# Kernel tuning notes

Hardware: AMD Instinct MI355X
Metric: run time of the kernel (lower is better)

## Reference

```python
import jax, jax.numpy as jnp
import numpy as np

B, C, F = 16384, 1000, 256
ALPHA = 10


def setup_inputs() -> dict:
    key = jax.random.key(0)
    k1, k2, k3, k4, k5 = jax.random.split(key, 5)
    logits = jax.random.normal(k1, (B, C), dtype=jnp.float32)
    features = jax.random.normal(k2, (B, F), dtype=jnp.float32)
    mean_vecs = jax.random.normal(k3, (C, F), dtype=jnp.float32)
    # Per-class Weibull (shape, loc, scale) as fit by scipy.weibull_min.fit.
    wb_shape = jax.random.uniform(k4, (C,), dtype=jnp.float32, minval=1.0, maxval=4.0)
    wb_loc = jnp.zeros((C,), dtype=jnp.float32)
    # typical tail distance for randn features/means is ~sqrt(2F) ~ 22.6
    wb_scale = jax.random.uniform(k5, (C,), dtype=jnp.float32, minval=10.0, maxval=25.0)
    return {"logits": logits, "features": features, "mean_vecs": mean_vecs,
            "wb_shape": wb_shape, "wb_loc": wb_loc, "wb_scale": wb_scale}


def reference(logits, features, mean_vecs, wb_shape, wb_loc, wb_scale):
    # Batched per-class Euclidean distances via the GEMM identity
    # ||f - m||^2 = ||f||^2 + ||m||^2 - 2 f.m  (avoids [B,C,F] intermediate).
    f2 = jnp.sum(features * features, axis=1, keepdims=True)        # [B,1]
    m2 = jnp.sum(mean_vecs * mean_vecs, axis=1)                     # [C]
    d2 = f2 + m2[None, :] - 2.0 * (features @ mean_vecs.T)          # [B,C]
    dist = jnp.sqrt(jnp.maximum(d2, 1e-12))                         # [B,C]
    # Analytic weibull_min CDF: 1 - exp(-((x - loc)/scale)^c), 0 for x <= loc.
    xp = (dist - wb_loc[None, :]) / wb_scale[None, :]
    pos = xp > 0
    xp_safe = jnp.where(pos, xp, 1.0)
    w = jnp.where(pos, 1.0 - jnp.exp(-(xp_safe ** wb_shape[None, :])), 0.0)
    # OpenMax reweighting + softmax (exp/sum-normalize as in the original).
    scores = logits * (1.0 - w ** ALPHA)                            # [B,C]
    return jax.nn.softmax(scores, axis=-1)
```

## Files before the change

### kernel.cpp

```cpp
#include <hip/hip_runtime.h>

#define NB 16384
#define NC 1000
#define NF 256
#define SE_STRIDE 1004

typedef _Float16 half8 __attribute__((ext_vector_type(8)));
typedef float f32x4 __attribute__((ext_vector_type(4)));

__global__ __launch_bounds__(256) void prep_kernel(
    const float* __restrict__ mean_vecs,
    const float* __restrict__ wb_shape,
    const float* __restrict__ wb_loc,
    const float* __restrict__ wb_scale,
    _Float16* __restrict__ m16f,
    float* __restrict__ pm2,
    float* __restrict__ psh,
    float* __restrict__ pli,
    float* __restrict__ pis)
{
    const int lane = threadIdx.x & 63;
    const int W = blockIdx.x * 4 + (threadIdx.x >> 6);

    if (W < 512) {
        const int gt = W >> 3, kk = W & 7;
        int cls = gt * 16 + (lane & 15);
        if (cls > NC - 1) cls = NC - 1;
        const float* src = mean_vecs + (size_t)cls * NF + kk * 32 + (lane >> 4) * 8;
        const float4 lo = *(const float4*)src;
        const float4 hi = *(const float4*)(src + 4);
        half8 h;
        h[0]=(_Float16)lo.x; h[1]=(_Float16)lo.y; h[2]=(_Float16)lo.z; h[3]=(_Float16)lo.w;
        h[4]=(_Float16)hi.x; h[5]=(_Float16)hi.y; h[6]=(_Float16)hi.z; h[7]=(_Float16)hi.w;
        *((half8*)m16f + (size_t)W * 64 + lane) = h;
    }
    if (W < NC) {
        const float4 v = *((const float4*)(mean_vecs + (size_t)W * NF) + lane);
        float s = v.x*v.x + v.y*v.y + v.z*v.z + v.w*v.w;
        #pragma unroll
        for (int off = 1; off < 64; off <<= 1) s += __shfl_xor(s, off, 64);
        if (lane == 0) {
            const float isc = 1.0f / wb_scale[W];
            pm2[W] = s;
            psh[W] = wb_shape[W];
            pli[W] = wb_loc[W] * isc;
            pis[W] = isc;
        }
    }
}

__global__ __launch_bounds__(512, 4) void score_kernel(
    const float* __restrict__ logits,
    const float* __restrict__ features,
    const _Float16* __restrict__ m16f,
    const float* __restrict__ pm2,
    const float* __restrict__ psh,
    const float* __restrict__ pli,
    const float* __restrict__ pis,
    float* __restrict__ out)
{
    __shared__ float se[16][SE_STRIDE];

    const int lane = threadIdx.x & 63;
    const int wave = threadIdx.x >> 6;
    const int q    = lane >> 4;
    const int mr   = lane & 15;
    const int row  = blockIdx.x * 16 + mr;

    const half8* mbase = (const half8*)m16f + (size_t)(wave * 8) * 8 * 64 + lane;

    half8 a[8];
    #pragma unroll
    for (int kk = 0; kk < 8; ++kk)
        a[kk] = mbase[kk * 64];

    half8 bfrag[8];
    float f2 = 0.f;
    const float* fb = features + (size_t)row * NF;
    #pragma unroll
    for (int kk = 0; kk < 8; ++kk) {
        const float4* p = (const float4*)(fb + kk * 32 + q * 8);
        const float4 lo = p[0], hi = p[1];
        f2 += lo.x*lo.x + lo.y*lo.y + lo.z*lo.z + lo.w*lo.w
            + hi.x*hi.x + hi.y*hi.y + hi.z*hi.z + hi.w*hi.w;
        half8 b;
        b[0]=(_Float16)lo.x; b[1]=(_Float16)lo.y; b[2]=(_Float16)lo.z; b[3]=(_Float16)lo.w;
        b[4]=(_Float16)hi.x; b[5]=(_Float16)hi.y; b[6]=(_Float16)hi.z; b[7]=(_Float16)hi.w;
        bfrag[kk] = b;
    }
    f2 += __shfl_xor(f2, 16, 64);
    f2 += __shfl_xor(f2, 32, 64);

    const float LOG2E = 1.44269504088896340736f;

    #pragma unroll
    for (int t = 0; t < 8; ++t) {
        const int gt   = wave * 8 + t;
        const int cb   = gt * 16 + q * 4;
        const bool cvg = (cb <= NC - 4);
        const int cbc  = cvg ? cb : (NC - 4);

        f32x4 acc = {0.f, 0.f, 0.f, 0.f};
        #pragma unroll
        for (int kk = 0; kk < 8; ++kk)
            acc = __builtin_amdgcn_mfma_f32_16x16x32_f16(a[kk], bfrag[kk], acc, 0, 0, 0);

        if (t < 7) {
            #pragma unroll
            for (int kk = 0; kk < 8; ++kk)
                a[kk] = mbase[(size_t)((t + 1) * 8 + kk) * 64];
        }

        const float4 m2v = *(const float4*)(pm2 + cbc);
        const float4 shv = *(const float4*)(psh + cbc);
        const float4 liv = *(const float4*)(pli + cbc);
        const float4 iv  = *(const float4*)(pis + cbc);

        const float* m2a = (const float*)&m2v;
        const float* sha = (const float*)&shv;
        const float* lia = (const float*)&liv;
        const float* iva = (const float*)&iv;

        f32x4 o;
        #pragma unroll
        for (int j = 0; j < 4; ++j) {
            float d2   = fmaxf(f2 + m2a[j] - 2.0f * acc[j], 1e-12f);
            float dist = sqrtf(d2);
            float xp   = dist * iva[j] - lia[j];
            float xs   = fmaxf(xp, 1e-30f);
            float tt   = exp2f(sha[j] * log2f(xs));
            float w    = 1.0f - exp2f(-LOG2E * tt);
            w = (xp > 0.f) ? w : 0.f;
            float w2 = w * w, w4 = w2 * w2, w8 = w4 * w4;
            o[j] = 1.0f - w8 * w2;
        }

        if (cvg)
            *(f32x4*)&se[mr][cb] = o;
    }

    __syncthreads();

    #pragma unroll
    for (int rr = 0; rr < 2; ++rr) {
        const int r = wave * 2 + rr;
        const size_t grow = (size_t)(blockIdx.x * 16 + r);
        const float* lrow = logits + grow * NC;

        float4 ev[4];
        float psum = 0.f;
        #pragma unroll
        for (int i = 0; i < 4; ++i) {
            const int idx = i * 64 + lane;
            if (idx < 250) {
                const float4 g4 = *(const float4*)&se[r][idx * 4];
                const float4 l4 = *(const float4*)(lrow + idx * 4);
                float4 e4;
                e4.x = exp2f(LOG2E * (l4.x * g4.x));
                e4.y = exp2f(LOG2E * (l4.y * g4.y));
                e4.z = exp2f(LOG2E * (l4.z * g4.z));
                e4.w = exp2f(LOG2E * (l4.w * g4.w));
                ev[i] = e4;
                psum += (e4.x + e4.y) + (e4.z + e4.w);
            }
        }
        #pragma unroll
        for (int off = 1; off < 64; off <<= 1)
            psum += __shfl_xor(psum, off, 64);
        const float inv = 1.0f / psum;

        float* orow = out + grow * NC;
        #pragma unroll
        for (int i = 0; i < 4; ++i) {
            const int idx = i * 64 + lane;
            if (idx < 250) {
                float4 v = ev[i];
                v.x *= inv; v.y *= inv; v.z *= inv; v.w *= inv;
                *(float4*)(orow + idx * 4) = v;
            }
        }
    }
}

extern "C" void kernel_launch(void* const* d_in, const int* in_sizes, int n_in,
                              void* d_out, int out_size, void* d_ws, size_t ws_size,
                              hipStream_t stream) {
    const float* logits    = (const float*)d_in[0];
    const float* features  = (const float*)d_in[1];
    const float* mean_vecs = (const float*)d_in[2];
    const float* wb_shape  = (const float*)d_in[3];
    const float* wb_loc    = (const float*)d_in[4];
    const float* wb_scale  = (const float*)d_in[5];
    float* out = (float*)d_out;

    _Float16* m16f = (_Float16*)d_ws;
    float* pm2 = (float*)((char*)d_ws + 524288);
    float* psh = (float*)((char*)d_ws + 524288 + 4096);
    float* pli = (float*)((char*)d_ws + 524288 + 8192);
    float* pis = (float*)((char*)d_ws + 524288 + 12288);

    prep_kernel<<<252, 256, 0, stream>>>(mean_vecs, wb_shape, wb_loc, wb_scale,
                                         m16f, pm2, psh, pli, pis);
    score_kernel<<<NB / 16, 512, 0, stream>>>(logits, features, m16f,
                                              pm2, psh, pli, pis, out);
}
```

Measured before the change: 170.8 us.

## Stage per-class params in LDS, split MFMA accumulators, prefetch logits before barrier

Copies the four per-class parameter arrays (m2, shape, loc/scale, 1/scale) into shared memory once per block so the epilogue reads LDS instead of global memory. Splits the MFMA accumulation into two independent chains to shorten the dependency chain. Issues the logits loads before the barrier so their latency overlaps the barrier and other waves' score computation. Costs 16KB extra LDS per block and more registers for the prefetched logits, which may reduce occupancy.

```diff
diff --git a/kernel.cpp b/kernel.cpp
--- a/kernel.cpp
+++ b/kernel.cpp
@@ -60,12 +60,25 @@
     float* __restrict__ out)
 {
     __shared__ float se[16][SE_STRIDE];
+    __shared__ float sp[4][1024];
 
     const int lane = threadIdx.x & 63;
     const int wave = threadIdx.x >> 6;
     const int q    = lane >> 4;
     const int mr   = lane & 15;
     const int row  = blockIdx.x * 16 + mr;
+
+    {
+        const int t = threadIdx.x;
+        if (t < 256) {
+            ((float4*)&sp[0][0])[t] = ((const float4*)pm2)[t];
+            ((float4*)&sp[2][0])[t] = ((const float4*)pli)[t];
+        } else {
+            const int u = t - 256;
+            ((float4*)&sp[1][0])[u] = ((const float4*)psh)[u];
+            ((float4*)&sp[3][0])[u] = ((const float4*)pis)[u];
+        }
+    }
 
     const half8* mbase = (const half8*)m16f + (size_t)(wave * 8) * 8 * 64 + lane;
 
@@ -91,6 +104,8 @@
     f2 += __shfl_xor(f2, 16, 64);
     f2 += __shfl_xor(f2, 32, 64);
 
+    __syncthreads();
+
     const float LOG2E = 1.44269504088896340736f;
 
     #pragma unroll
@@ -100,10 +115,13 @@
         const bool cvg = (cb <= NC - 4);
         const int cbc  = cvg ? cb : (NC - 4);
 
-        f32x4 acc = {0.f, 0.f, 0.f, 0.f};
-        #pragma unroll
-        for (int kk = 0; kk < 8; ++kk)
-            acc = __builtin_amdgcn_mfma_f32_16x16x32_f16(a[kk], bfrag[kk], acc, 0, 0, 0);
+        f32x4 acc0 = {0.f, 0.f, 0.f, 0.f};
+        f32x4 acc1 = {0.f, 0.f, 0.f, 0.f};
+        #pragma unroll
+        for (int kk = 0; kk < 4; ++kk) {
+            acc0 = __builtin_amdgcn_mfma_f32_16x16x32_f16(a[kk],     bfrag[kk],     acc0, 0, 0, 0);
+            acc1 = __builtin_amdgcn_mfma_f32_16x16x32_f16(a[kk + 4], bfrag[kk + 4], acc1, 0, 0, 0);
+        }
 
         if (t < 7) {
             #pragma unroll
@@ -111,24 +129,20 @@
                 a[kk] = mbase[(size_t)((t + 1) * 8 + kk) * 64];
         }
 
-        const float4 m2v = *(const float4*)(pm2 + cbc);
-        const float4 shv = *(const float4*)(psh + cbc);
-        const float4 liv = *(const float4*)(pli + cbc);
-        const float4 iv  = *(const float4*)(pis + cbc);
-
-        const float* m2a = (const float*)&m2v;
-        const float* sha = (const float*)&shv;
-        const float* lia = (const float*)&liv;
-        const float* iva = (const float*)&iv;
+        const f32x4 m2v = *(const f32x4*)&sp[0][cbc];
+        const f32x4 shv = *(const f32x4*)&sp[1][cbc];
+        const f32x4 liv = *(const f32x4*)&sp[2][cbc];
+        const f32x4 iv  = *(const f32x4*)&sp[3][cbc];
 
         f32x4 o;
         #pragma unroll
         for (int j = 0; j < 4; ++j) {
-            float d2   = fmaxf(f2 + m2a[j] - 2.0f * acc[j], 1e-12f);
+            float av   = acc0[j] + acc1[j];
+            float d2   = fmaxf(f2 + m2v[j] - 2.0f * av, 1e-12f);
             float dist = sqrtf(d2);
-            float xp   = dist * iva[j] - lia[j];
+            float xp   = dist * iv[j] - liv[j];
             float xs   = fmaxf(xp, 1e-30f);
-            float tt   = exp2f(sha[j] * log2f(xs));
+            float tt   = exp2f(shv[j] * log2f(xs));
             float w    = 1.0f - exp2f(-LOG2E * tt);
             w = (xp > 0.f) ? w : 0.f;
             float w2 = w * w, w4 = w2 * w2, w8 = w4 * w4;
@@ -139,13 +153,24 @@
             *(f32x4*)&se[mr][cb] = o;
     }
 
+    float4 lgp[2][4];
+    #pragma unroll
+    for (int rr = 0; rr < 2; ++rr) {
+        const size_t grow = (size_t)(blockIdx.x * 16 + wave * 2 + rr);
+        const float* lrow = logits + grow * NC;
+        #pragma unroll
+        for (int i = 0; i < 4; ++i) {
+            const int idx = i * 64 + lane;
+            if (idx < 250) lgp[rr][i] = *(const float4*)(lrow + idx * 4);
+        }
+    }
+
     __syncthreads();
 
     #pragma unroll
     for (int rr = 0; rr < 2; ++rr) {
         const int r = wave * 2 + rr;
         const size_t grow = (size_t)(blockIdx.x * 16 + r);
-        const float* lrow = logits + grow * NC;
 
         float4 ev[4];
         float psum = 0.f;
@@ -154,7 +179,7 @@
             const int idx = i * 64 + lane;
             if (idx < 250) {
                 const float4 g4 = *(const float4*)&se[r][idx * 4];
-                const float4 l4 = *(const float4*)(lrow + idx * 4);
+                const float4 l4 = lgp[rr][i];
                 float4 e4;
                 e4.x = exp2f(LOG2E * (l4.x * g4.x));
                 e4.y = exp2f(LOG2E * (l4.y * g4.y));
```

Result: faster. 163.1 us (-4.5%).
